# Kernel tuning notes

Hardware: AMD Instinct MI355X
Metric: run time of the kernel (lower is better)

Reference implementation:

```python
import jax, jax.numpy as jnp
import numpy as np

N = 100000  # nodes per answer graph
E = 3200000  # edges per answer graph
D = 300  # GloVe embedding dim
H = 16  # hidden dim


def gcn_conv(x, src, dst, W, b):
    """PyG-style GCNConv: add self-loops, symmetric norm, aggregate at target."""
    n = x.shape[0]
    loops = jnp.arange(n, dtype=src.dtype)
    s = jnp.concatenate([src, loops])  # [E+N]
    d = jnp.concatenate([dst, loops])
    deg = jnp.zeros((n,), x.dtype).at[d].add(1.0)
    dis = jnp.where(deg > 0, jax.lax.rsqrt(deg), 0.0)  # deg^{-1/2}
    h = x @ W  # [N, out]
    norm = dis[s] * dis[d]  # [E+N]
    msg = h[s] * norm[:, None]
    agg = jax.ops.segment_sum(msg, d, num_segments=n)
    return agg + b


def _one_answer(x, ei, W1, b1, W2, b2):
    src, dst = ei[0], ei[1]
    h = jax.nn.relu(gcn_conv(x, src, dst, W1, b1))
    # dropout omitted (eval mode: F.dropout(training=False) is identity)
    out = gcn_conv(h, src, dst, W2, b2)  # [N, 1]
    return out.mean()


def setup_inputs() -> dict:
    key = jax.random.key(0)
    k1, k2, k3, k4 = jax.random.split(key, 4)
    emb = jax.random.normal(k1, (5, N, D), jnp.float32)
    edge_index = jax.random.randint(k2, (5, 2, E), 0, N, jnp.int64)
    W1 = jax.random.normal(k3, (D, H), jnp.float32) * (1.0 / np.sqrt(D))
    b1 = jnp.zeros((H,), jnp.float32)
    W2 = jax.random.normal(k4, (H, 1), jnp.float32) * (1.0 / np.sqrt(H))
    b2 = jnp.zeros((1,), jnp.float32)
    return {"emb": emb, "edge_index": edge_index, "W1": W1, "b1": b1, "W2": W2, "b2": b2}


def reference(emb, edge_index, W1, b1, W2, b2):
    scores = jax.vmap(_one_answer, in_axes=(0, 0, None, None, None, None))(
        emb, edge_index, W1, b1, W2, b2)  # [5]
    return jax.nn.softmax(scores, axis=0)
```

## Files before the change

### kernel.cpp

```cpp
#include <hip/hip_runtime.h>
#include <hip/hip_bf16.h>

#define N_ 100000
#define E_ 3200000
#define DIM 300
#define HID 16
#define NGRAPH 5
#define NB 196
#define BSH 9
#define BNODES 512
#define CAP 20480
#define SCAP 24576

__device__ __forceinline__ void fatomic(float* p, float v) { unsafeAtomicAdd(p, v); }

__global__ __launch_bounds__(256) void bucket_kernel(const int* __restrict__ ei,
                                                     unsigned* __restrict__ bcur,
                                                     unsigned* __restrict__ bedge) {
    int g = blockIdx.y;
    const int4* src4 = (const int4*)(ei + (size_t)g * 2 * E_);
    const int4* dst4 = (const int4*)(ei + (size_t)g * 2 * E_ + E_);
    unsigned* bc = bcur + (size_t)g * NB;
    unsigned* be = bedge + (size_t)g * NB * CAP;
    __shared__ unsigned hist[NB], curs[NB];
    int tid = threadIdx.x;
    const int CHUNK = 4096;
    const int nchunk = (E_ + CHUNK - 1) / CHUNK;
    for (int c = blockIdx.x; c < nchunk; c += gridDim.x) {
        int cb = c * CHUNK;
        for (int i = tid; i < NB; i += 256) hist[i] = 0u;
        __syncthreads();
        int4 sv[4], dv[4]; bool val[4];
#pragma unroll
        for (int k = 0; k < 4; ++k) {
            int e0 = cb + k * 1024 + tid * 4;
            val[k] = (e0 < E_);
            if (val[k]) { sv[k] = src4[e0 >> 2]; dv[k] = dst4[e0 >> 2]; }
        }
#pragma unroll
        for (int k = 0; k < 4; ++k) if (val[k]) {
            atomicAdd(&hist[((unsigned)dv[k].x) >> BSH], 1u);
            atomicAdd(&hist[((unsigned)dv[k].y) >> BSH], 1u);
            atomicAdd(&hist[((unsigned)dv[k].z) >> BSH], 1u);
            atomicAdd(&hist[((unsigned)dv[k].w) >> BSH], 1u);
        }
        __syncthreads();
        for (int i = tid; i < NB; i += 256) curs[i] = atomicAdd(&bc[i], hist[i]);
        __syncthreads();
#define EMIT(S, D) { unsigned bb = ((unsigned)(D)) >> BSH; \
        unsigned pos = atomicAdd(&curs[bb], 1u); \
        if (pos < CAP) be[(size_t)bb * CAP + pos] = (((unsigned)(S)) << BSH) | (((unsigned)(D)) & (BNODES - 1)); }
#pragma unroll
        for (int k = 0; k < 4; ++k) if (val[k]) {
            EMIT(sv[k].x, dv[k].x)
            EMIT(sv[k].y, dv[k].y)
            EMIT(sv[k].z, dv[k].z)
            EMIT(sv[k].w, dv[k].w)
        }
#undef EMIT
        __syncthreads();
    }
}

__global__ __launch_bounds__(256) void sortb_kernel(const unsigned* __restrict__ bcur,
                                                    const unsigned* __restrict__ bedge,
                                                    unsigned* __restrict__ ssrc,
                                                    unsigned* __restrict__ offA,
                                                    unsigned* __restrict__ degA,
                                                    float* __restrict__ dis) {
    int g = blockIdx.y, b = blockIdx.x;
    __shared__ unsigned hist[BNODES], offL[BNODES], curL[BNODES], part[256];
    int tid = threadIdx.x;
    hist[tid] = 0u; hist[tid + 256] = 0u;
    __syncthreads();
    unsigned n = bcur[(size_t)g * NB + b]; if (n > CAP) n = CAP;
    const unsigned* beb = bedge + ((size_t)g * NB + b) * CAP;
    for (unsigned i = tid; i < n; i += 256) atomicAdd(&hist[beb[i] & (BNODES - 1)], 1u);
    __syncthreads();
    unsigned d0 = hist[2 * tid], d1 = hist[2 * tid + 1];
    unsigned p0 = (d0 + 7u) & ~7u, p1 = (d1 + 7u) & ~7u;
    part[tid] = p0 + p1;
    __syncthreads();
    for (int o = 1; o < 256; o <<= 1) {
        unsigned v = (tid >= o) ? part[tid - o] : 0u;
        __syncthreads();
        part[tid] += v;
        __syncthreads();
    }
    unsigned base = part[tid] - p0 - p1;
    offL[2 * tid] = base;     curL[2 * tid] = base;
    offL[2 * tid + 1] = base + p0; curL[2 * tid + 1] = base + p0;
    int node0 = b << BSH;
    unsigned sbase = (unsigned)(((size_t)g * NB + b) * SCAP);
    float* disg = dis + (size_t)g * N_;
    unsigned* offg = offA + (size_t)g * (NB << BSH);
    unsigned* degg = degA + (size_t)g * (NB << BSH);
    {
        int i = 2 * tid, node = node0 + i;
        offg[node] = sbase + offL[i]; degg[node] = d0;
        if (node < N_) disg[node] = rsqrtf((float)d0 + 1.0f);
        i = 2 * tid + 1; node = node0 + i;
        offg[node] = sbase + offL[i]; degg[node] = d1;
        if (node < N_) disg[node] = rsqrtf((float)d1 + 1.0f);
    }
    __syncthreads();
    for (unsigned i = tid; i < n; i += 256) {
        unsigned pk = beb[i];
        unsigned pos = atomicAdd(&curL[pk & (BNODES - 1)], 1u);
        ssrc[(size_t)sbase + pos] = pk >> BSH;
    }
}

#define FMA4(acc, sv, wv) \
    acc.x += (sv) * (wv).x; acc.y += (sv) * (wv).y; acc.z += (sv) * (wv).z; acc.w += (sv) * (wv).w;

__global__ __launch_bounds__(256) void gemm_kernel(const float* __restrict__ x,
                                                   const float* __restrict__ W1,
                                                   const float* __restrict__ dis,
                                                   float* __restrict__ hd, int ntot) {
    __shared__ float wsh[DIM * HID];
    for (int i = threadIdx.x; i < DIM * HID; i += blockDim.x) wsh[i] = W1[i];
    __syncthreads();
    int node = blockIdx.x * blockDim.x + threadIdx.x;
    if (node >= ntot) return;
    const float4* xr = (const float4*)(x + (size_t)node * DIM);
    float4 a0 = {0,0,0,0}, a1 = {0,0,0,0}, a2 = {0,0,0,0}, a3 = {0,0,0,0};
    float4 q0, q1, q2, q3;
#define STEP(XS, B) \
    q0 = wr[(B)+0]; q1 = wr[(B)+1]; q2 = wr[(B)+2]; q3 = wr[(B)+3]; \
    FMA4(a0, XS, q0) FMA4(a1, XS, q1) FMA4(a2, XS, q2) FMA4(a3, XS, q3)
#pragma unroll 3
    for (int k4 = 0; k4 < DIM / 4; ++k4) {
        float4 xv = xr[k4];
        const float4* wr = (const float4*)(wsh + k4 * 4 * HID);
        STEP(xv.x, 0)
        STEP(xv.y, 4)
        STEP(xv.z, 8)
        STEP(xv.w, 12)
    }
#undef STEP
    float dn = dis[node];
    a0.x *= dn; a0.y *= dn; a0.z *= dn; a0.w *= dn;
    a1.x *= dn; a1.y *= dn; a1.z *= dn; a1.w *= dn;
    a2.x *= dn; a2.y *= dn; a2.z *= dn; a2.w *= dn;
    a3.x *= dn; a3.y *= dn; a3.z *= dn; a3.w *= dn;
    float4* hr = (float4*)(hd + (size_t)node * HID);
    hr[0] = a0; hr[1] = a1; hr[2] = a2; hr[3] = a3;
}

__global__ __launch_bounds__(512) void bagg_kernel(const unsigned* __restrict__ ssrc,
                                                   const unsigned* __restrict__ offA,
                                                   const unsigned* __restrict__ degA,
                                                   const float* __restrict__ hd,
                                                   const float* __restrict__ dis,
                                                   const float* __restrict__ b1,
                                                   const float* __restrict__ W2,
                                                   float* __restrict__ t_) {
    int g = blockIdx.y, b = blockIdx.x;
    const float* hdg = hd + (size_t)g * N_ * HID;
    const float* disg = dis + (size_t)g * N_;
    const unsigned* offg = offA + (size_t)g * (NB << BSH);
    const unsigned* degg = degA + (size_t)g * (NB << BSH);
    float* tg = t_ + (size_t)g * N_;
    int tid = threadIdx.x, j = tid & 15, sub = tid >> 4;
    float b1j = b1[j], w2j = W2[j];
    int node0 = b << BSH;
#pragma unroll 1
    for (int m = 0; m < 16; ++m) {
        int node = node0 + sub + (m << 5);
        if (node >= N_) continue;
        unsigned k0 = offg[node], dg = degg[node];
        float acc = hdg[(size_t)node * HID + j];
        unsigned k = 0;
        for (; k + 8 <= dg; k += 8) {
            const int4* ip = (const int4*)(ssrc + k0 + k);
            int4 i0 = ip[0], i1 = ip[1];
            float v0 = hdg[(size_t)(unsigned)i0.x * HID + j];
            float v1 = hdg[(size_t)(unsigned)i0.y * HID + j];
            float v2 = hdg[(size_t)(unsigned)i0.z * HID + j];
            float v3 = hdg[(size_t)(unsigned)i0.w * HID + j];
            float v4 = hdg[(size_t)(unsigned)i1.x * HID + j];
            float v5 = hdg[(size_t)(unsigned)i1.y * HID + j];
            float v6 = hdg[(size_t)(unsigned)i1.z * HID + j];
            float v7 = hdg[(size_t)(unsigned)i1.w * HID + j];
            acc += ((v0 + v1) + (v2 + v3)) + ((v4 + v5) + (v6 + v7));
        }
        for (; k < dg; ++k) acc += hdg[(size_t)ssrc[k0 + k] * HID + j];
        float dn = disg[node];
        float val = fmaxf(acc * dn + b1j, 0.f) * w2j;
        val += __shfl_xor(val, 1);
        val += __shfl_xor(val, 2);
        val += __shfl_xor(val, 4);
        val += __shfl_xor(val, 8);
        if (j == 0) tg[node] = val * dn;
    }
}

__global__ __launch_bounds__(256) void score_kernel(const int* __restrict__ ei,
                                                    const float* __restrict__ t_,
                                                    const float* __restrict__ dis,
                                                    float* __restrict__ S) {
    int g = blockIdx.y;
    const int4* src4 = (const int4*)(ei + (size_t)g * 2 * E_);
    const int4* dst4 = (const int4*)(ei + (size_t)g * 2 * E_ + E_);
    const float* tg = t_ + (size_t)g * N_;
    const float* disg = dis + (size_t)g * N_;
    float c = 0.f;
    int stride = gridDim.x * blockDim.x;
    int gid = blockIdx.x * blockDim.x + threadIdx.x;
    for (int e = gid; e < E_ / 4; e += stride) {
        int4 sv = src4[e];
        int4 dv = dst4[e];
        c += tg[sv.x] * disg[dv.x];
        c += tg[sv.y] * disg[dv.y];
        c += tg[sv.z] * disg[dv.z];
        c += tg[sv.w] * disg[dv.w];
    }
    for (int i = gid; i < N_; i += stride) c += tg[i] * disg[i];
    for (int o = 32; o > 0; o >>= 1) c += __shfl_down(c, o);
    __shared__ float red[4];
    int wid = threadIdx.x >> 6, lane = threadIdx.x & 63;
    if (lane == 0) red[wid] = c;
    __syncthreads();
    if (threadIdx.x == 0) fatomic(&S[g], red[0] + red[1] + red[2] + red[3]);
}

__global__ void final_kernel(const float* __restrict__ S, const float* __restrict__ b2,
                             float* __restrict__ out) {
    if (threadIdx.x == 0) {
        float sc[NGRAPH];
        float m = -1e30f;
        for (int g = 0; g < NGRAPH; ++g) {
            sc[g] = b2[0] + S[g] * (1.0f / N_);
            m = fmaxf(m, sc[g]);
        }
        float sum = 0.f;
        for (int g = 0; g < NGRAPH; ++g) { sc[g] = expf(sc[g] - m); sum += sc[g]; }
        for (int g = 0; g < NGRAPH; ++g) out[g] = sc[g] / sum;
    }
}

extern "C" void kernel_launch(void* const* d_in, const int* in_sizes, int n_in,
                              void* d_out, int out_size, void* d_ws, size_t ws_size,
                              hipStream_t stream) {
    const float* emb = (const float*)d_in[0];
    const int* ei    = (const int*)d_in[1];
    const float* W1  = (const float*)d_in[2];
    const float* b1  = (const float*)d_in[3];
    const float* W2  = (const float*)d_in[4];
    const float* b2  = (const float*)d_in[5];
    float* out = (float*)d_out;

    float* S = (float*)d_ws;
    unsigned* bcurAll = (unsigned*)((char*)d_ws + 256);
    size_t hdr = 256 + (size_t)NGRAPH * NB * 4;
    hdr = (hdr + 255) & ~(size_t)255;
    char* base = (char*)d_ws + hdr;
    size_t avail = (ws_size > hdr) ? ws_size - hdr : 0;

    size_t sz_be   = (size_t)NB * CAP * 4;
    size_t sz_ss   = (size_t)NB * SCAP * 4;
    size_t sz_off  = (size_t)(NB << BSH) * 4;
    size_t sz_hd   = (size_t)N_ * HID * 4;
    size_t sz_dis  = (size_t)N_ * 4;
    size_t sz_t    = (size_t)N_ * 4;
    size_t per = sz_be + sz_ss + 2 * sz_off + sz_hd + sz_dis + sz_t + 1024;
    int maxChunk = (int)(avail / per);
    if (maxChunk > NGRAPH) maxChunk = NGRAPH;
    if (maxChunk < 1) maxChunk = 1;

    hipMemsetAsync(d_ws, 0, 256 + (size_t)NGRAPH * NB * 4, stream);

    for (int g0 = 0; g0 < NGRAPH; g0 += maxChunk) {
        int ng = (NGRAPH - g0 < maxChunk) ? (NGRAPH - g0) : maxChunk;
        char* p = base;
        unsigned* bedge = (unsigned*)p; p += (size_t)ng * sz_be;
        unsigned* ssrc  = (unsigned*)p; p += (size_t)ng * sz_ss;
        unsigned* offA  = (unsigned*)p; p += (size_t)ng * sz_off;
        unsigned* degA  = (unsigned*)p; p += (size_t)ng * sz_off;
        float* hd  = (float*)p; p += (size_t)ng * sz_hd;
        float* dis = (float*)p; p += (size_t)ng * sz_dis;
        float* t_  = (float*)p;
        unsigned* bcur = bcurAll + (size_t)g0 * NB;

        const int* eic  = ei  + (size_t)g0 * 2 * E_;
        const float* xc = emb + (size_t)g0 * N_ * DIM;

        bucket_kernel<<<dim3(128, ng), 256, 0, stream>>>(eic, bcur, bedge);
        sortb_kernel<<<dim3(NB, ng), 256, 0, stream>>>(bcur, bedge, ssrc, offA, degA, dis);
        gemm_kernel<<<dim3((ng * N_ + 255) / 256), 256, 0, stream>>>(xc, W1, dis, hd, ng * N_);
        bagg_kernel<<<dim3(NB, ng), 512, 0, stream>>>(ssrc, offA, degA, hd, dis, b1, W2, t_);
        score_kernel<<<dim3(512, ng), 256, 0, stream>>>(eic, t_, dis, S + g0);
    }
    final_kernel<<<1, 64, 0, stream>>>(S, b2, out);
}
```

Baseline: 925.0 us.

## Split hidden features into two cache-sized halves and compute score from CSR

```diff
diff --git a/kernel.cpp b/kernel.cpp
--- a/kernel.cpp
+++ b/kernel.cpp
@@ -144,8 +144,11 @@
     a1.x *= dn; a1.y *= dn; a1.z *= dn; a1.w *= dn;
     a2.x *= dn; a2.y *= dn; a2.z *= dn; a2.w *= dn;
     a3.x *= dn; a3.y *= dn; a3.z *= dn; a3.w *= dn;
-    float4* hr = (float4*)(hd + (size_t)node * HID);
-    hr[0] = a0; hr[1] = a1; hr[2] = a2; hr[3] = a3;
+    int gi = node / N_, local = node - gi * N_;
+    float4* h0 = (float4*)(hd + (size_t)gi * N_ * HID + (size_t)local * 8);
+    float4* h1 = (float4*)(hd + (size_t)gi * N_ * HID + (size_t)N_ * 8 + (size_t)local * 8);
+    h0[0] = a0; h0[1] = a1;
+    h1[0] = a2; h1[1] = a3;
 }
 
 __global__ __launch_bounds__(512) void bagg_kernel(const unsigned* __restrict__ ssrc,
@@ -155,74 +158,85 @@
                                                    const float* __restrict__ dis,
                                                    const float* __restrict__ b1,
                                                    const float* __restrict__ W2,
-                                                   float* __restrict__ t_) {
+                                                   float* __restrict__ t_, int half) {
     int g = blockIdx.y, b = blockIdx.x;
-    const float* hdg = hd + (size_t)g * N_ * HID;
+    const float* hdh = hd + (size_t)g * N_ * HID + (size_t)half * N_ * 8;
     const float* disg = dis + (size_t)g * N_;
     const unsigned* offg = offA + (size_t)g * (NB << BSH);
     const unsigned* degg = degA + (size_t)g * (NB << BSH);
     float* tg = t_ + (size_t)g * N_;
-    int tid = threadIdx.x, j = tid & 15, sub = tid >> 4;
-    float b1j = b1[j], w2j = W2[j];
+    int tid = threadIdx.x, j = tid & 7, grp = tid >> 3;
+    float b1j = b1[half * 8 + j], w2j = W2[half * 8 + j];
     int node0 = b << BSH;
 #pragma unroll 1
-    for (int m = 0; m < 16; ++m) {
-        int node = node0 + sub + (m << 5);
+    for (int m = 0; m < 8; ++m) {
+        int node = node0 + grp + (m << 6);
         if (node >= N_) continue;
         unsigned k0 = offg[node], dg = degg[node];
-        float acc = hdg[(size_t)node * HID + j];
+        float acc = hdh[(size_t)node * 8 + j];
         unsigned k = 0;
         for (; k + 8 <= dg; k += 8) {
             const int4* ip = (const int4*)(ssrc + k0 + k);
             int4 i0 = ip[0], i1 = ip[1];
-            float v0 = hdg[(size_t)(unsigned)i0.x * HID + j];
-            float v1 = hdg[(size_t)(unsigned)i0.y * HID + j];
-            float v2 = hdg[(size_t)(unsigned)i0.z * HID + j];
-            float v3 = hdg[(size_t)(unsigned)i0.w * HID + j];
-            float v4 = hdg[(size_t)(unsigned)i1.x * HID + j];
-            float v5 = hdg[(size_t)(unsigned)i1.y * HID + j];
-            float v6 = hdg[(size_t)(unsigned)i1.z * HID + j];
-            float v7 = hdg[(size_t)(unsigned)i1.w * HID + j];
+            float v0 = hdh[(size_t)(unsigned)i0.x * 8 + j];
+            float v1 = hdh[(size_t)(unsigned)i0.y * 8 + j];
+            float v2 = hdh[(size_t)(unsigned)i0.z * 8 + j];
+            float v3 = hdh[(size_t)(unsigned)i0.w * 8 + j];
+            float v4 = hdh[(size_t)(unsigned)i1.x * 8 + j];
+            float v5 = hdh[(size_t)(unsigned)i1.y * 8 + j];
+            float v6 = hdh[(size_t)(unsigned)i1.z * 8 + j];
+            float v7 = hdh[(size_t)(unsigned)i1.w * 8 + j];
             acc += ((v0 + v1) + (v2 + v3)) + ((v4 + v5) + (v6 + v7));
         }
-        for (; k < dg; ++k) acc += hdg[(size_t)ssrc[k0 + k] * HID + j];
+        for (; k < dg; ++k) acc += hdh[(size_t)ssrc[k0 + k] * 8 + j];
         float dn = disg[node];
         float val = fmaxf(acc * dn + b1j, 0.f) * w2j;
         val += __shfl_xor(val, 1);
         val += __shfl_xor(val, 2);
         val += __shfl_xor(val, 4);
-        val += __shfl_xor(val, 8);
-        if (j == 0) tg[node] = val * dn;
-    }
-}
-
-__global__ __launch_bounds__(256) void score_kernel(const int* __restrict__ ei,
-                                                    const float* __restrict__ t_,
-                                                    const float* __restrict__ dis,
-                                                    float* __restrict__ S) {
-    int g = blockIdx.y;
-    const int4* src4 = (const int4*)(ei + (size_t)g * 2 * E_);
-    const int4* dst4 = (const int4*)(ei + (size_t)g * 2 * E_ + E_);
+        if (j == 0) {
+            float o = val * dn;
+            if (half == 0) tg[node] = o;
+            else tg[node] += o;
+        }
+    }
+}
+
+__global__ __launch_bounds__(512) void score2_kernel(const unsigned* __restrict__ ssrc,
+                                                     const unsigned* __restrict__ offA,
+                                                     const unsigned* __restrict__ degA,
+                                                     const float* __restrict__ t_,
+                                                     const float* __restrict__ dis,
+                                                     float* __restrict__ S) {
+    int g = blockIdx.y, b = blockIdx.x;
     const float* tg = t_ + (size_t)g * N_;
     const float* disg = dis + (size_t)g * N_;
+    const unsigned* offg = offA + (size_t)g * (NB << BSH);
+    const unsigned* degg = degA + (size_t)g * (NB << BSH);
+    int tid = threadIdx.x, j = tid & 3, grp = tid >> 2;
+    int node0 = b << BSH;
     float c = 0.f;
-    int stride = gridDim.x * blockDim.x;
-    int gid = blockIdx.x * blockDim.x + threadIdx.x;
-    for (int e = gid; e < E_ / 4; e += stride) {
-        int4 sv = src4[e];
-        int4 dv = dst4[e];
-        c += tg[sv.x] * disg[dv.x];
-        c += tg[sv.y] * disg[dv.y];
-        c += tg[sv.z] * disg[dv.z];
-        c += tg[sv.w] * disg[dv.w];
-    }
-    for (int i = gid; i < N_; i += stride) c += tg[i] * disg[i];
+#pragma unroll 1
+    for (int m = 0; m < 4; ++m) {
+        int node = node0 + grp + (m << 7);
+        if (node >= N_) continue;
+        unsigned k0 = offg[node], dg = degg[node];
+        float acc = 0.f;
+        for (unsigned k = j; k < dg; k += 4) acc += tg[ssrc[k0 + k]];
+        acc += __shfl_xor(acc, 1);
+        acc += __shfl_xor(acc, 2);
+        if (j == 0) c += disg[node] * (acc + tg[node]);
+    }
     for (int o = 32; o > 0; o >>= 1) c += __shfl_down(c, o);
-    __shared__ float red[4];
-    int wid = threadIdx.x >> 6, lane = threadIdx.x & 63;
+    __shared__ float red[8];
+    int wid = tid >> 6, lane = tid & 63;
     if (lane == 0) red[wid] = c;
     __syncthreads();
-    if (threadIdx.x == 0) fatomic(&S[g], red[0] + red[1] + red[2] + red[3]);
+    if (tid == 0) {
+        float s = 0.f;
+        for (int w = 0; w < 8; ++w) s += red[w];
+        fatomic(&S[g], s);
+    }
 }
 
 __global__ void final_kernel(const float* __restrict__ S, const float* __restrict__ b2,
@@ -289,8 +303,9 @@
         bucket_kernel<<<dim3(128, ng), 256, 0, stream>>>(eic, bcur, bedge);
         sortb_kernel<<<dim3(NB, ng), 256, 0, stream>>>(bcur, bedge, ssrc, offA, degA, dis);
         gemm_kernel<<<dim3((ng * N_ + 255) / 256), 256, 0, stream>>>(xc, W1, dis, hd, ng * N_);
-        bagg_kernel<<<dim3(NB, ng), 512, 0, stream>>>(ssrc, offA, degA, hd, dis, b1, W2, t_);
-        score_kernel<<<dim3(512, ng), 256, 0, stream>>>(eic, t_, dis, S + g0);
+        bagg_kernel<<<dim3(NB, ng), 512, 0, stream>>>(ssrc, offA, degA, hd, dis, b1, W2, t_, 0);
+        bagg_kernel<<<dim3(NB, ng), 512, 0, stream>>>(ssrc, offA, degA, hd, dis, b1, W2, t_, 1);
+        score2_kernel<<<dim3(NB, ng), 512, 0, stream>>>(ssrc, offA, degA, t_, dis, S + g0);
     }
     final_kernel<<<1, 64, 0, stream>>>(S, b2, out);
 }
```

After: 1.088 ms. 1.18x slower.
